# Kernel optimization log

Measured on AMD Instinct MI355X. Metric: run time of the kernel, lower is better.

## Reference

```python
import jax, jax.numpy as jnp
import numpy as np

B, C, N = 4, 128, 25000
E = 200000            # edges per graph
H, DH = 4, 32         # heads, per-head dim
OUT = H * DH          # 128
ED = 32               # edge feature dim


def setup_inputs() -> dict:
    key = jax.random.key(0)
    ks = jax.random.split(key, 16)
    s = 0.05
    return {
        'x': jax.random.normal(ks[0], (B, C, N, 1), jnp.float32),
        'edge_index': jax.random.randint(ks[1], (B, 2, E), 0, B * N, jnp.int64),
        'edge_attr': jax.random.normal(ks[2], (B * E, ED), jnp.float32),
        'Wq': jax.random.normal(ks[3], (C, OUT), jnp.float32) * s,
        'bq': jnp.zeros((OUT,), jnp.float32),
        'Wk': jax.random.normal(ks[4], (C, OUT), jnp.float32) * s,
        'bk': jnp.zeros((OUT,), jnp.float32),
        'Wv': jax.random.normal(ks[5], (C, OUT), jnp.float32) * s,
        'bv': jnp.zeros((OUT,), jnp.float32),
        'We': jax.random.normal(ks[6], (ED, OUT), jnp.float32) * s,
        'Wskip': jax.random.normal(ks[7], (C, OUT), jnp.float32) * s,
        'bskip': jnp.zeros((OUT,), jnp.float32),
        'W1': jax.random.normal(ks[8], (OUT, 2 * OUT), jnp.float32) * s,
        'b1': jnp.zeros((2 * OUT,), jnp.float32),
        'W2': jax.random.normal(ks[9], (2 * OUT, OUT), jnp.float32) * s,
        'b2': jnp.zeros((OUT,), jnp.float32),
    }


def reference(x, edge_index, edge_attr, Wq, bq, Wk, bk, Wv, bv, We,
              Wskip, bskip, W1, b1, W2, b2):
    b, c, n, _ = x.shape
    nb = b * n
    # [B,C,N,1] -> [B*N, C]
    xf = x.squeeze(-1).transpose(0, 2, 1).reshape(nb, c)
    # [B,2,E] -> [2, B*E]
    ei = edge_index.transpose(1, 0, 2).reshape(2, -1)
    src, dst = ei[0], ei[1]

    q = (xf @ Wq + bq).reshape(nb, H, DH)
    k = (xf @ Wk + bk).reshape(nb, H, DH)
    v = (xf @ Wv + bv).reshape(nb, H, DH)
    e = (edge_attr @ We).reshape(-1, H, DH)  # [T,H,DH]

    qi = q[dst]            # gather target queries  [T,H,DH]
    kj = k[src] + e        # gather source keys + edge proj
    vj = v[src] + e

    scale = 1.0 / np.sqrt(DH).astype(np.float32)
    alpha = (qi * kj).sum(-1) * scale  # [T,H]

    # segment softmax over edges sharing a destination node
    amax = jax.ops.segment_max(alpha, dst, num_segments=nb)
    amax = jnp.where(jnp.isfinite(amax), amax, 0.0)
    ea = jnp.exp(alpha - amax[dst])
    denom = jax.ops.segment_sum(ea, dst, num_segments=nb)
    attn = ea / (denom[dst] + 1e-16)   # [T,H]

    agg = jax.ops.segment_sum(vj * attn[..., None], dst, num_segments=nb)
    out = agg.reshape(nb, OUT) + (xf @ Wskip + bskip)  # root skip

    # feed-forward + final activation
    h = jnp.maximum(out @ W1 + b1, 0.0) @ W2 + b2
    h = jnp.maximum(h, 0.0)

    # [B*N, OUT] -> [B, OUT, N, 1]
    return h.reshape(b, n, OUT).transpose(0, 2, 1)[..., None]
```

## Files before the change

### kernel.cpp

```cpp
#include <hip/hip_runtime.h>
#include <hip/hip_bf16.h>

#define NB      100000
#define NPB     25000
#define T_E     800000
#define EPG     200000
#define DMODEL  128
#define EDIM    32
#define FFD     256
#define SCAN_NBLK 98
#define PROJ_BLK  1563
#define HIST_BLK  3125
#define EPROJ_BLK 2048

typedef __attribute__((ext_vector_type(8))) short bf16x8;
typedef __attribute__((ext_vector_type(4))) float f32x4;
typedef __attribute__((ext_vector_type(2))) float f32x2;

__device__ inline unsigned short f2bf(float f) {
    unsigned u = __float_as_uint(f);
    unsigned r = u + 0x7fffu + ((u >> 16) & 1u);
    return (unsigned short)(r >> 16);
}
__device__ inline unsigned pack_bf16x2(float lo, float hi) {
    return (unsigned)f2bf(lo) | ((unsigned)f2bf(hi) << 16);
}
__device__ inline float bf_lo(unsigned p) { return __uint_as_float(p << 16); }
__device__ inline float bf_hi(unsigned p) { return __uint_as_float(p & 0xffff0000u); }

__global__ __launch_bounds__(256) void k_prep(
    const float* __restrict__ W1, const float* __restrict__ W2,
    const float* __restrict__ We,
    const float* __restrict__ Wq, const float* __restrict__ Wk,
    const float* __restrict__ Wv, const float* __restrict__ Wskip,
    uint4* __restrict__ w1f, uint4* __restrict__ w2f,
    uint4* __restrict__ wef, uint4* __restrict__ wpf)
{
    int t = blockIdx.x * 256 + threadIdx.x;
    int lane = t & 63;
    int frag = t >> 6;
    if (frag >= 264) return;
    int rl = lane & 15, g = lane >> 4;
    unsigned v[4];
    if (frag < 64) {
        int m1 = frag >> 2, ks = frag & 3;
        int col1 = m1 * 16 + rl;
        int k0 = ks * 32 + g * 8;
#pragma unroll
        for (int j2 = 0; j2 < 4; ++j2) {
            float f0 = W1[(k0 + 2 * j2) * FFD + col1];
            float f1 = W1[(k0 + 2 * j2 + 1) * FFD + col1];
            v[j2] = pack_bf16x2(f0, f1);
        }
        w1f[frag * 64 + lane] = make_uint4(v[0], v[1], v[2], v[3]);
    } else if (frag < 128) {
        int f2 = frag - 64;
        int m2 = f2 >> 3, ks = f2 & 7;
        int c2 = m2 * 16 + rl;
        int k0 = ks * 32 + g * 8;
#pragma unroll
        for (int j2 = 0; j2 < 4; ++j2) {
            float f0 = W2[(k0 + 2 * j2) * DMODEL + c2];
            float f1 = W2[(k0 + 2 * j2 + 1) * DMODEL + c2];
            v[j2] = pack_bf16x2(f0, f1);
        }
        w2f[f2 * 64 + lane] = make_uint4(v[0], v[1], v[2], v[3]);
    } else if (frag < 136) {
        int m = frag - 128;
        int ocol = m * 16 + rl;
        int k0 = g * 8;
#pragma unroll
        for (int j2 = 0; j2 < 4; ++j2) {
            float f0 = We[(k0 + 2 * j2) * DMODEL + ocol];
            float f1 = We[(k0 + 2 * j2 + 1) * DMODEL + ocol];
            v[j2] = pack_bf16x2(f0, f1);
        }
        wef[m * 64 + lane] = make_uint4(v[0], v[1], v[2], v[3]);
    } else {
        int fi = frag - 136;
        int m  = fi >> 5;
        int r  = fi & 31;
        int ct = r >> 2, ks = r & 3;
        const float* W = (m == 0) ? Wq : (m == 1) ? Wk : (m == 2) ? Wv : Wskip;
        int col = ct * 16 + rl;
        int k0  = ks * 32 + g * 8;
#pragma unroll
        for (int j2 = 0; j2 < 4; ++j2) {
            float f0 = W[(k0 + 2 * j2) * DMODEL + col];
            float f1 = W[(k0 + 2 * j2 + 1) * DMODEL + col];
            v[j2] = pack_bf16x2(f0, f1);
        }
        wpf[fi * 64 + lane] = make_uint4(v[0], v[1], v[2], v[3]);
    }
}

#define STG 16384

__global__ __launch_bounds__(256) void k_projhist(
    const float* __restrict__ x, const uint4* __restrict__ wpf,
    const float* __restrict__ bq, const float* __restrict__ bk,
    const float* __restrict__ bv, const float* __restrict__ bskip,
    unsigned short* __restrict__ qb16, unsigned short* __restrict__ kvb,
    unsigned short* __restrict__ skipb16,
    const int* __restrict__ eidx, int* __restrict__ counts)
{
    __shared__ __align__(16) char lds[32768];
    const int tid = threadIdx.x;

    if (blockIdx.x >= PROJ_BLK) {
        int t = (blockIdx.x - PROJ_BLK) * 256 + tid;
        if (t < T_E) {
            int b = t / EPG, e = t - b * EPG;
            int dst = eidx[(size_t)(b * 2 + 1) * EPG + e];
            atomicAdd(&counts[dst], 1);
        }
        return;
    }

    const int node0 = blockIdx.x * 64;

    {
        const int nl   = tid & 63;
        const int half = tid >> 6;
        const int node = node0 + nl;
        const bool valid = node < NB;
        int b  = node / NPB;
        int nn = node - b * NPB;
        const float* xbase = x + (size_t)b * DMODEL * NPB + nn;
#pragma unroll
        for (int o = 0; o < 4; ++o) {
            int c0 = (half * 4 + o) * 8;
            unsigned vals[4];
#pragma unroll
            for (int j2 = 0; j2 < 4; ++j2) {
                float f0 = valid ? xbase[(size_t)(c0 + 2 * j2) * NPB] : 0.f;
                float f1 = valid ? xbase[(size_t)(c0 + 2 * j2 + 1) * NPB] : 0.f;
                vals[j2] = pack_bf16x2(f0, f1);
            }
            int byte = nl * 256 + ((c0 * 2) ^ ((nl & 7) << 4));
            *(uint4*)(&lds[byte]) = make_uint4(vals[0], vals[1], vals[2], vals[3]);
        }
    }
    __syncthreads();

    const int w = tid >> 6, lane = tid & 63;
    const int rl = lane & 15, g = lane >> 4;

    for (int m = 0; m < 4; ++m) {
        const float* bi = (m == 0) ? bq : (m == 1) ? bk : (m == 2) ? bv : bskip;
#pragma unroll
        for (int ct2 = 0; ct2 < 2; ++ct2) {
            const int ct = w * 2 + ct2;
            bf16x8 A[4];
#pragma unroll
            for (int ks = 0; ks < 4; ++ks)
                A[ks] = *(const bf16x8*)&wpf[((m * 8 + ct) * 4 + ks) * 64 + lane];
            const int colb = ct * 16 + g * 4;
            const float bb0 = bi[colb], bb1 = bi[colb + 1],
                        bb2 = bi[colb + 2], bb3 = bi[colb + 3];
#pragma unroll
            for (int nt = 0; nt < 4; ++nt) {
                const int nl = nt * 16 + rl;
                f32x4 acc = {0.f, 0.f, 0.f, 0.f};
#pragma unroll
                for (int ks = 0; ks < 4; ++ks) {
                    bf16x8 B = *(const bf16x8*)(&lds[nl * 256 +
                                  ((ks * 64 + g * 16) ^ ((nl & 7) << 4))]);
                    acc = __builtin_amdgcn_mfma_f32_16x16x32_bf16(A[ks], B, acc, 0, 0, 0);
                }
                unsigned lo = pack_bf16x2(acc[0] + bb0, acc[1] + bb1);
                unsigned hi = pack_bf16x2(acc[2] + bb2, acc[3] + bb3);
                int byte = STG + nl * 256 + ((colb * 2) ^ ((nl & 7) << 4));
                *(uint2*)(&lds[byte]) = make_uint2(lo, hi);
            }
        }
        __syncthreads();
#pragma unroll
        for (int i = 0; i < 4; ++i) {
            int linear = i * 256 + tid;
            int row = linear >> 4;
            int c8  = (linear & 15) * 8;
            int node = node0 + row;
            if (node < NB) {
                uint4 vv = *(const uint4*)(&lds[STG + row * 256 +
                                ((c8 * 2) ^ ((row & 7) << 4))]);
                if (m == 0)      *(uint4*)&qb16[(size_t)node * DMODEL + c8] = vv;
                else if (m == 1) *(uint4*)&kvb[(size_t)node * 256 + c8] = vv;
                else if (m == 2) *(uint4*)&kvb[(size_t)node * 256 + 128 + c8] = vv;
                else             *(uint4*)&skipb16[(size_t)node * DMODEL + c8] = vv;
            }
        }
        __syncthreads();
    }
}

__global__ __launch_bounds__(1024) void k_scan1(
    const int* __restrict__ counts, int* __restrict__ row_start,
    int* __restrict__ bsum)
{
    __shared__ int s[1024];
    const int tid = threadIdx.x;
    const int gid = blockIdx.x * 1024 + tid;
    int v = (gid < NB) ? counts[gid] : 0;
    s[tid] = v;
    __syncthreads();
#pragma unroll
    for (int off = 1; off < 1024; off <<= 1) {
        int tv = (tid >= off) ? s[tid - off] : 0;
        __syncthreads();
        s[tid] += tv;
        __syncthreads();
    }
    int incl = s[tid];
    if (gid < NB) row_start[gid] = incl - v;
    if (tid == 1023) bsum[blockIdx.x] = incl;
}

__global__ __launch_bounds__(128) void k_scan2(int* __restrict__ bsum)
{
    __shared__ int s[128];
    const int tid = threadIdx.x;
    int v = (tid < SCAN_NBLK) ? bsum[tid] : 0;
    s[tid] = v;
    __syncthreads();
#pragma unroll
    for (int off = 1; off < 128; off <<= 1) {
        int tv = (tid >= off) ? s[tid - off] : 0;
        __syncthreads();
        s[tid] += tv;
        __syncthreads();
    }
    if (tid < SCAN_NBLK) bsum[tid] = s[tid] - v;
}

__global__ __launch_bounds__(1024) void k_scan3(
    int* __restrict__ row_start, const int* __restrict__ bsum,
    int* __restrict__ cursor)
{
    const int gid = blockIdx.x * 1024 + threadIdx.x;
    if (gid < NB) {
        int v = row_start[gid] + bsum[blockIdx.x];
        row_start[gid] = v;
        cursor[gid] = v;
    }
}

__global__ __launch_bounds__(256) void k_escat2(
    const float* __restrict__ eattr, const uint4* __restrict__ wef,
    unsigned char* __restrict__ eb,
    const int* __restrict__ eidx, int* __restrict__ cursor,
    int2* __restrict__ elist2)
{
    __shared__ __align__(16) char elds[8192];
    const int tid = threadIdx.x;

    if (blockIdx.x >= EPROJ_BLK) {
        int t = (blockIdx.x - EPROJ_BLK) * 256 + tid;
        if (t < T_E) {
            int b = t / EPG, e = t - b * EPG;
            int dst = eidx[(size_t)(b * 2 + 1) * EPG + e];
            int src = eidx[(size_t)(b * 2) * EPG + e];
            int pos = atomicAdd(&cursor[dst], 1);
            elist2[pos] = make_int2(src, t);
        }
        return;
    }

    const int w = tid >> 6, lane = tid & 63;
    const int rl = lane & 15, g = lane >> 4;
    char* myl = &elds[w * 2048];

    bf16x8 a[8];
#pragma unroll
    for (int m = 0; m < 8; ++m) a[m] = *(const bf16x8*)&wef[m * 64 + lane];

    const int nwaves = EPROJ_BLK * 4;
    for (int tile = blockIdx.x * 4 + w; tile < T_E / 16; tile += nwaves) {
        const float* ep = &eattr[((size_t)tile * 16 + rl) * EDIM + g * 8];
        float4 f0 = *(const float4*)ep;
        float4 f1 = *(const float4*)(ep + 4);
        uint4 bu = make_uint4(pack_bf16x2(f0.x, f0.y), pack_bf16x2(f0.z, f0.w),
                              pack_bf16x2(f1.x, f1.y), pack_bf16x2(f1.z, f1.w));
        bf16x8 b = *(bf16x8*)&bu;
        f32x4 z = {0.f, 0.f, 0.f, 0.f};
        f32x4 acc[8];
#pragma unroll
        for (int m = 0; m < 8; ++m)
            acc[m] = __builtin_amdgcn_mfma_f32_16x16x32_bf16(a[m], b, z, 0, 0, 0);
#pragma unroll
        for (int m = 0; m < 8; ++m) {
            unsigned d = __builtin_amdgcn_cvt_pk_fp8_f32(acc[m][0], acc[m][1], 0, false);
            d = __builtin_amdgcn_cvt_pk_fp8_f32(acc[m][2], acc[m][3], d, true);
            *(unsigned*)(myl + rl * 128 + ((m * 16) ^ ((rl & 7) << 4)) + g * 4) = d;
        }
#pragma unroll
        for (int it = 0; it < 2; ++it) {
            int lin = it * 64 + lane;
            int row = lin >> 3, chunk = lin & 7;
            uint4 vv = *(const uint4*)(myl + row * 128 + ((chunk ^ (row & 7)) << 4));
            *(uint4*)&eb[(size_t)tile * 2048 + (size_t)lin * 16] = vv;
        }
    }
}

__global__ __launch_bounds__(256) void k_aggr3(
    unsigned short* qx,
    const unsigned short* __restrict__ kvb,
    const unsigned short* __restrict__ skipb16,
    const unsigned char* __restrict__ eb,
    const int2* __restrict__ elist2,
    const int* __restrict__ row_start, const int* __restrict__ row_end)
{
    const int tid = threadIdx.x;
    const int w = tid >> 6, l = tid & 63;
    const int q4 = l >> 4;
    const int li = l & 15;
    const int c0 = li * 8;

    const int nwaves = gridDim.x * 4;
    for (int node = blockIdx.x * 4 + w; node < NB; node += nwaves) {
        const int rs = row_start[node];
        const int re = row_end[node];
        uint4 qp = *(const uint4*)&qx[(size_t)node * DMODEL + c0];
        const float q0 = bf_lo(qp.x), q1 = bf_hi(qp.x);
        const float q2 = bf_lo(qp.y), q3 = bf_hi(qp.y);
        const float q4_ = bf_lo(qp.z), q5 = bf_hi(qp.z);
        const float q6 = bf_lo(qp.w), q7 = bf_hi(qp.w);
        float a0 = 0.f, a1 = 0.f, a2 = 0.f, a3 = 0.f;
        float a4 = 0.f, a5 = 0.f, a6 = 0.f, a7 = 0.f, den = 0.f;

        for (int j0 = rs; j0 < re; j0 += 8) {
            const int jcA = j0 + q4;
            const int jcB = j0 + 4 + q4;
            const bool actA = jcA < re;
            const bool actB = jcB < re;
            uint4 kpA = make_uint4(0,0,0,0), vpA = make_uint4(0,0,0,0);
            uint4 kpB = make_uint4(0,0,0,0), vpB = make_uint4(0,0,0,0);
            uint2 epA = make_uint2(0,0), epB = make_uint2(0,0);
            if (actA) {
                int2 se = elist2[jcA];
                kpA = *(const uint4*)&kvb[(size_t)se.x * 256 + c0];
                vpA = *(const uint4*)&kvb[(size_t)se.x * 256 + 128 + c0];
                epA = *(const uint2*)&eb[(size_t)se.y * DMODEL + c0];
            }
            if (actB) {
                int2 se = elist2[jcB];
                kpB = *(const uint4*)&kvb[(size_t)se.x * 256 + c0];
                vpB = *(const uint4*)&kvb[(size_t)se.x * 256 + 128 + c0];
                epB = *(const uint2*)&eb[(size_t)se.y * DMODEL + c0];
            }
            {
                f32x2 exl = __builtin_amdgcn_cvt_pk_f32_fp8(epA.x, false);
                f32x2 exh = __builtin_amdgcn_cvt_pk_f32_fp8(epA.x, true);
                f32x2 eyl = __builtin_amdgcn_cvt_pk_f32_fp8(epA.y, false);
                f32x2 eyh = __builtin_amdgcn_cvt_pk_f32_fp8(epA.y, true);
                const float e0 = exl[0], e1 = exl[1], e2 = exh[0], e3 = exh[1];
                const float e4 = eyl[0], e5 = eyl[1], e6 = eyh[0], e7 = eyh[1];
                float p = q0 * (bf_lo(kpA.x) + e0) + q1 * (bf_hi(kpA.x) + e1)
                        + q2 * (bf_lo(kpA.y) + e2) + q3 * (bf_hi(kpA.y) + e3)
                        + q4_ * (bf_lo(kpA.z) + e4) + q5 * (bf_hi(kpA.z) + e5)
                        + q6 * (bf_lo(kpA.w) + e6) + q7 * (bf_hi(kpA.w) + e7);
                p += __shfl_xor(p, 1, 64);
                p += __shfl_xor(p, 2, 64);
                float ea = actA ? __expf(p * 0.17677669529663689f) : 0.f;
                a0 += ea * (bf_lo(vpA.x) + e0);  a1 += ea * (bf_hi(vpA.x) + e1);
                a2 += ea * (bf_lo(vpA.y) + e2);  a3 += ea * (bf_hi(vpA.y) + e3);
                a4 += ea * (bf_lo(vpA.z) + e4);  a5 += ea * (bf_hi(vpA.z) + e5);
                a6 += ea * (bf_lo(vpA.w) + e6);  a7 += ea * (bf_hi(vpA.w) + e7);
                den += ea;
            }
            {
                f32x2 exl = __builtin_amdgcn_cvt_pk_f32_fp8(epB.x, false);
                f32x2 exh = __builtin_amdgcn_cvt_pk_f32_fp8(epB.x, true);
                f32x2 eyl = __builtin_amdgcn_cvt_pk_f32_fp8(epB.y, false);
                f32x2 eyh = __builtin_amdgcn_cvt_pk_f32_fp8(epB.y, true);
                const float e0 = exl[0], e1 = exl[1], e2 = exh[0], e3 = exh[1];
                const float e4 = eyl[0], e5 = eyl[1], e6 = eyh[0], e7 = eyh[1];
                float p = q0 * (bf_lo(kpB.x) + e0) + q1 * (bf_hi(kpB.x) + e1)
                        + q2 * (bf_lo(kpB.y) + e2) + q3 * (bf_hi(kpB.y) + e3)
                        + q4_ * (bf_lo(kpB.z) + e4) + q5 * (bf_hi(kpB.z) + e5)
                        + q6 * (bf_lo(kpB.w) + e6) + q7 * (bf_hi(kpB.w) + e7);
                p += __shfl_xor(p, 1, 64);
                p += __shfl_xor(p, 2, 64);
                float ea = actB ? __expf(p * 0.17677669529663689f) : 0.f;
                a0 += ea * (bf_lo(vpB.x) + e0);  a1 += ea * (bf_hi(vpB.x) + e1);
                a2 += ea * (bf_lo(vpB.y) + e2);  a3 += ea * (bf_hi(vpB.y) + e3);
                a4 += ea * (bf_lo(vpB.z) + e4);  a5 += ea * (bf_hi(vpB.z) + e5);
                a6 += ea * (bf_lo(vpB.w) + e6);  a7 += ea * (bf_hi(vpB.w) + e7);
                den += ea;
            }
        }
#pragma unroll
        for (int off = 16; off <= 32; off <<= 1) {
            a0 += __shfl_xor(a0, off, 64);  a1 += __shfl_xor(a1, off, 64);
            a2 += __shfl_xor(a2, off, 64);  a3 += __shfl_xor(a3, off, 64);
            a4 += __shfl_xor(a4, off, 64);  a5 += __shfl_xor(a5, off, 64);
            a6 += __shfl_xor(a6, off, 64);  a7 += __shfl_xor(a7, off, 64);
            den += __shfl_xor(den, off, 64);
        }
        float r = 1.0f / (den + 1e-16f);
        if (q4 == 0) {
            uint4 sp = *(const uint4*)&skipb16[(size_t)node * DMODEL + c0];
            uint4 o;
            o.x = pack_bf16x2(a0 * r + bf_lo(sp.x), a1 * r + bf_hi(sp.x));
            o.y = pack_bf16x2(a2 * r + bf_lo(sp.y), a3 * r + bf_hi(sp.y));
            o.z = pack_bf16x2(a4 * r + bf_lo(sp.z), a5 * r + bf_hi(sp.z));
            o.w = pack_bf16x2(a6 * r + bf_lo(sp.w), a7 * r + bf_hi(sp.w));
            *(uint4*)&qx[(size_t)node * DMODEL + c0] = o;
        }
    }
}

#define H1_OFF 16384

__global__ __launch_bounds__(256) void k_ffn_mfma(
    const unsigned short* __restrict__ xs16,
    const uint4* __restrict__ w1f, const float* __restrict__ b1,
    const uint4* __restrict__ w2f, const float* __restrict__ b2,
    float* __restrict__ out)
{
    __shared__ __align__(16) char lds[49152];
    const int tid   = threadIdx.x;
    const int node0 = blockIdx.x * 64;

#pragma unroll
    for (int i = 0; i < 4; ++i) {
        int linear = i * 256 + tid;
        int row = linear >> 4;
        int c8  = (linear & 15) * 8;
        int node = node0 + row;
        uint4 vv = (node < NB) ? *(const uint4*)&xs16[(size_t)node * DMODEL + c8]
                               : make_uint4(0, 0, 0, 0);
        int byte = row * 256 + ((c8 * 2) ^ ((row & 7) << 4));
        *(uint4*)(&lds[byte]) = vv;
    }
    __syncthreads();

    const int w = tid >> 6, lane = tid & 63;
    const int rl = lane & 15, g = lane >> 4;

    {
        f32x4 acc[4][4] = {};
#pragma unroll
        for (int ks = 0; ks < 4; ++ks) {
            bf16x8 a[4], b[4];
#pragma unroll
            for (int mt = 0; mt < 4; ++mt) {
                int m1 = w * 4 + mt;
                a[mt] = *(const bf16x8*)&w1f[(m1 * 4 + ks) * 64 + lane];
            }
#pragma unroll
            for (int nt = 0; nt < 4; ++nt) {
                int node = nt * 16 + rl;
                int byte = node * 256 + ((ks * 64 + g * 16) ^ ((node & 7) << 4));
                b[nt] = *(const bf16x8*)&lds[byte];
            }
#pragma unroll
            for (int mt = 0; mt < 4; ++mt)
#pragma unroll
                for (int nt = 0; nt < 4; ++nt)
                    acc[mt][nt] = __builtin_amdgcn_mfma_f32_16x16x32_bf16(
                        a[mt], b[nt], acc[mt][nt], 0, 0, 0);
        }
#pragma unroll
        for (int mt = 0; mt < 4; ++mt) {
            int col1_0 = w * 64 + mt * 16 + g * 4;
            float bb0 = b1[col1_0], bb1 = b1[col1_0 + 1],
                  bb2 = b1[col1_0 + 2], bb3 = b1[col1_0 + 3];
#pragma unroll
            for (int nt = 0; nt < 4; ++nt) {
                int node = nt * 16 + rl;
                float v0 = fmaxf(acc[mt][nt][0] + bb0, 0.f);
                float v1 = fmaxf(acc[mt][nt][1] + bb1, 0.f);
                float v2 = fmaxf(acc[mt][nt][2] + bb2, 0.f);
                float v3 = fmaxf(acc[mt][nt][3] + bb3, 0.f);
                unsigned lo = pack_bf16x2(v0, v1), hi = pack_bf16x2(v2, v3);
                int byte = H1_OFF + node * 512 + ((col1_0 * 2) ^ ((node & 7) << 4));
                *(uint2*)(&lds[byte]) = make_uint2(lo, hi);
            }
        }
    }
    __syncthreads();

    {
        f32x4 acc[2][4] = {};
#pragma unroll
        for (int ks = 0; ks < 8; ++ks) {
            bf16x8 a[2], b[4];
#pragma unroll
            for (int mt = 0; mt < 2; ++mt) {
                int m2 = w * 2 + mt;
                a[mt] = *(const bf16x8*)&w2f[(m2 * 8 + ks) * 64 + lane];
            }
#pragma unroll
            for (int nt = 0; nt < 4; ++nt) {
                int node = nt * 16 + rl;
                int byte = H1_OFF + node * 512 + ((ks * 64 + g * 16) ^ ((node & 7) << 4));
                b[nt] = *(const bf16x8*)&lds[byte];
            }
#pragma unroll
            for (int mt = 0; mt < 2; ++mt)
#pragma unroll
                for (int nt = 0; nt < 4; ++nt)
                    acc[mt][nt] = __builtin_amdgcn_mfma_f32_16x16x32_bf16(
                        a[mt], b[nt], acc[mt][nt], 0, 0, 0);
        }
#pragma unroll
        for (int mt = 0; mt < 2; ++mt) {
            int c2_0 = w * 32 + mt * 16 + g * 4;
#pragma unroll
            for (int nt = 0; nt < 4; ++nt) {
                int node = node0 + nt * 16 + rl;
                if (node < NB) {
                    int bb = node / NPB;
                    int nn = node - bb * NPB;
                    size_t base = (size_t)(bb * DMODEL) * NPB + nn;
#pragma unroll
                    for (int r = 0; r < 4; ++r) {
                        float v = fmaxf(acc[mt][nt][r] + b2[c2_0 + r], 0.f);
                        out[base + (size_t)(c2_0 + r) * NPB] = v;
                    }
                }
            }
        }
    }
}

extern "C" void kernel_launch(void* const* d_in, const int* in_sizes, int n_in,
                              void* d_out, int out_size, void* d_ws, size_t ws_size,
                              hipStream_t stream)
{
    const float* x     = (const float*)d_in[0];
    const int*   eidx  = (const int*)  d_in[1];
    const float* eattr = (const float*)d_in[2];
    const float* Wq    = (const float*)d_in[3];
    const float* bq    = (const float*)d_in[4];
    const float* Wk    = (const float*)d_in[5];
    const float* bk    = (const float*)d_in[6];
    const float* Wv    = (const float*)d_in[7];
    const float* bv    = (const float*)d_in[8];
    const float* We    = (const float*)d_in[9];
    const float* Wskip = (const float*)d_in[10];
    const float* bskip = (const float*)d_in[11];
    const float* W1    = (const float*)d_in[12];
    const float* b1    = (const float*)d_in[13];
    const float* W2    = (const float*)d_in[14];
    const float* b2    = (const float*)d_in[15];
    float* out = (float*)d_out;

    const size_t NBD = (size_t)NB * DMODEL;
    unsigned short* qb16    = (unsigned short*)d_ws;
    unsigned short* kvb     = qb16 + NBD;
    unsigned short* skipb16 = kvb + 2 * NBD;
    unsigned char*  eb      = (unsigned char*)(skipb16 + NBD);
    uint4* w1f = (uint4*)(eb + (size_t)T_E * DMODEL);
    uint4* w2f = w1f + 64 * 64;
    uint4* wef = w2f + 64 * 64;
    uint4* wpf = wef + 8 * 64;
    int* counts    = (int*)(wpf + 128 * 64);
    int* row_start = counts + NB;
    int* cursor    = row_start + NB;
    int2* elist2   = (int2*)(cursor + NB);
    int* bsum      = (int*)(elist2 + T_E);

    hipMemsetAsync(counts, 0, NB * sizeof(int), stream);
    k_prep<<<66, 256, 0, stream>>>(W1, W2, We, Wq, Wk, Wv, Wskip,
                                   w1f, w2f, wef, wpf);
    k_projhist<<<PROJ_BLK + HIST_BLK, 256, 0, stream>>>(
        x, wpf, bq, bk, bv, bskip, qb16, kvb, skipb16, eidx, counts);
    k_scan1<<<SCAN_NBLK, 1024, 0, stream>>>(counts, row_start, bsum);
    k_scan2<<<1, 128, 0, stream>>>(bsum);
    k_scan3<<<SCAN_NBLK, 1024, 0, stream>>>(row_start, bsum, cursor);
    k_escat2<<<EPROJ_BLK + HIST_BLK, 256, 0, stream>>>(
        eattr, wef, eb, eidx, cursor, elist2);
    k_aggr3<<<2048, 256, 0, stream>>>(qb16, kvb, skipb16, eb, elist2,
                                      row_start, cursor);
    k_ffn_mfma<<<(NB + 63) / 64, 256, 0, stream>>>(qb16, w1f, b1, w2f, b2, out);
}
```

Measured before the change: 306.5 us.

## Move edge-feature projection into node-projection/histogram kernel with interleaved block roles

The edge-attribute projection (MFMA to fp8) moves out of the scatter kernel into the first phase kernel, which now assigns node projection, edge projection and histogram work to blocks interleaved by blockIdx modulo 4. The scatter kernel becomes a plain atomic-cursor scatter. The edge projection loop also prefetches the next tile's attributes one iteration ahead. The aim is to overlap the bandwidth-heavy edge projection with the node projection and histogram, which do not depend on the prefix scan, and to shorten the serial chain after the scan. The cost is a larger fused launch with many early-exit blocks and a more complex role-dispatch kernel.

```diff
diff --git a/kernel.cpp b/kernel.cpp
--- a/kernel.cpp
+++ b/kernel.cpp
@@ -10,8 +10,9 @@
 #define FFD     256
 #define SCAN_NBLK 98
 #define PROJ_BLK  1563
-#define HIST_BLK  3125
-#define EPROJ_BLK 2048
+#define NT_E      50000
+#define PHA_GRP   1584
+#define PHA_BLK   (PHA_GRP * 4)
 
 typedef __attribute__((ext_vector_type(8))) short bf16x8;
 typedef __attribute__((ext_vector_type(4))) float f32x4;
@@ -96,19 +97,23 @@
 
 #define STG 16384
 
-__global__ __launch_bounds__(256) void k_projhist(
+__global__ __launch_bounds__(256) void k_phaseA(
     const float* __restrict__ x, const uint4* __restrict__ wpf,
     const float* __restrict__ bq, const float* __restrict__ bk,
     const float* __restrict__ bv, const float* __restrict__ bskip,
     unsigned short* __restrict__ qb16, unsigned short* __restrict__ kvb,
     unsigned short* __restrict__ skipb16,
+    const float* __restrict__ eattr, const uint4* __restrict__ wef,
+    unsigned char* __restrict__ eb,
     const int* __restrict__ eidx, int* __restrict__ counts)
 {
     __shared__ __align__(16) char lds[32768];
-    const int tid = threadIdx.x;
-
-    if (blockIdx.x >= PROJ_BLK) {
-        int t = (blockIdx.x - PROJ_BLK) * 256 + tid;
+    const int tid  = threadIdx.x;
+    const int role = blockIdx.x & 3;
+
+    if (role >= 2) {
+        int hid = (blockIdx.x >> 2) * 2 + (blockIdx.x & 1);
+        int t = hid * 256 + tid;
         if (t < T_E) {
             int b = t / EPG, e = t - b * EPG;
             int dst = eidx[(size_t)(b * 2 + 1) * EPG + e];
@@ -117,7 +122,60 @@
         return;
     }
 
-    const int node0 = blockIdx.x * 64;
+    const int w = tid >> 6, lane = tid & 63;
+    const int rl = lane & 15, g = lane >> 4;
+
+    if (role == 1) {
+        char* myl = &lds[w * 2048];
+        bf16x8 a[8];
+#pragma unroll
+        for (int m = 0; m < 8; ++m) a[m] = *(const bf16x8*)&wef[m * 64 + lane];
+
+        const int stride = PHA_GRP * 4;
+        int tile = (blockIdx.x >> 2) * 4 + w;
+        if (tile >= NT_E) return;
+        const float* ep = &eattr[((size_t)tile * 16 + rl) * EDIM + g * 8];
+        float4 f0 = *(const float4*)ep;
+        float4 f1 = *(const float4*)(ep + 4);
+        while (tile < NT_E) {
+            int tnext = tile + stride;
+            float4 nf0, nf1;
+            if (tnext < NT_E) {
+                const float* np = &eattr[((size_t)tnext * 16 + rl) * EDIM + g * 8];
+                nf0 = *(const float4*)np;
+                nf1 = *(const float4*)(np + 4);
+            }
+            uint4 bu = make_uint4(pack_bf16x2(f0.x, f0.y), pack_bf16x2(f0.z, f0.w),
+                                  pack_bf16x2(f1.x, f1.y), pack_bf16x2(f1.z, f1.w));
+            bf16x8 b = *(bf16x8*)&bu;
+            f32x4 z = {0.f, 0.f, 0.f, 0.f};
+            f32x4 acc[8];
+#pragma unroll
+            for (int m = 0; m < 8; ++m)
+                acc[m] = __builtin_amdgcn_mfma_f32_16x16x32_bf16(a[m], b, z, 0, 0, 0);
+#pragma unroll
+            for (int m = 0; m < 8; ++m) {
+                unsigned d = __builtin_amdgcn_cvt_pk_fp8_f32(acc[m][0], acc[m][1], 0, false);
+                d = __builtin_amdgcn_cvt_pk_fp8_f32(acc[m][2], acc[m][3], d, true);
+                *(unsigned*)(myl + rl * 128 + ((m * 16) ^ ((rl & 7) << 4)) + g * 4) = d;
+            }
+#pragma unroll
+            for (int it = 0; it < 2; ++it) {
+                int lin = it * 64 + lane;
+                int row = lin >> 3, chunk = lin & 7;
+                uint4 vv = *(const uint4*)(myl + row * 128 + ((chunk ^ (row & 7)) << 4));
+                *(uint4*)&eb[(size_t)tile * 2048 + (size_t)lin * 16] = vv;
+            }
+            tile = tnext;
+            f0 = nf0;
+            f1 = nf1;
+        }
+        return;
+    }
+
+    const int pid = blockIdx.x >> 2;
+    if (pid >= PROJ_BLK) return;
+    const int node0 = pid * 64;
 
     {
         const int nl   = tid & 63;
@@ -142,9 +200,6 @@
         }
     }
     __syncthreads();
-
-    const int w = tid >> 6, lane = tid & 63;
-    const int rl = lane & 15, g = lane >> 4;
 
     for (int m = 0; m < 4; ++m) {
         const float* bi = (m == 0) ? bq : (m == 1) ? bk : (m == 2) ? bv : bskip;
@@ -245,61 +300,17 @@
     }
 }
 
-__global__ __launch_bounds__(256) void k_escat2(
-    const float* __restrict__ eattr, const uint4* __restrict__ wef,
-    unsigned char* __restrict__ eb,
+__global__ __launch_bounds__(256) void k_scatter(
     const int* __restrict__ eidx, int* __restrict__ cursor,
     int2* __restrict__ elist2)
 {
-    __shared__ __align__(16) char elds[8192];
-    const int tid = threadIdx.x;
-
-    if (blockIdx.x >= EPROJ_BLK) {
-        int t = (blockIdx.x - EPROJ_BLK) * 256 + tid;
-        if (t < T_E) {
-            int b = t / EPG, e = t - b * EPG;
-            int dst = eidx[(size_t)(b * 2 + 1) * EPG + e];
-            int src = eidx[(size_t)(b * 2) * EPG + e];
-            int pos = atomicAdd(&cursor[dst], 1);
-            elist2[pos] = make_int2(src, t);
-        }
-        return;
-    }
-
-    const int w = tid >> 6, lane = tid & 63;
-    const int rl = lane & 15, g = lane >> 4;
-    char* myl = &elds[w * 2048];
-
-    bf16x8 a[8];
-#pragma unroll
-    for (int m = 0; m < 8; ++m) a[m] = *(const bf16x8*)&wef[m * 64 + lane];
-
-    const int nwaves = EPROJ_BLK * 4;
-    for (int tile = blockIdx.x * 4 + w; tile < T_E / 16; tile += nwaves) {
-        const float* ep = &eattr[((size_t)tile * 16 + rl) * EDIM + g * 8];
-        float4 f0 = *(const float4*)ep;
-        float4 f1 = *(const float4*)(ep + 4);
-        uint4 bu = make_uint4(pack_bf16x2(f0.x, f0.y), pack_bf16x2(f0.z, f0.w),
-                              pack_bf16x2(f1.x, f1.y), pack_bf16x2(f1.z, f1.w));
-        bf16x8 b = *(bf16x8*)&bu;
-        f32x4 z = {0.f, 0.f, 0.f, 0.f};
-        f32x4 acc[8];
-#pragma unroll
-        for (int m = 0; m < 8; ++m)
-            acc[m] = __builtin_amdgcn_mfma_f32_16x16x32_bf16(a[m], b, z, 0, 0, 0);
-#pragma unroll
-        for (int m = 0; m < 8; ++m) {
-            unsigned d = __builtin_amdgcn_cvt_pk_fp8_f32(acc[m][0], acc[m][1], 0, false);
-            d = __builtin_amdgcn_cvt_pk_fp8_f32(acc[m][2], acc[m][3], d, true);
-            *(unsigned*)(myl + rl * 128 + ((m * 16) ^ ((rl & 7) << 4)) + g * 4) = d;
-        }
-#pragma unroll
-        for (int it = 0; it < 2; ++it) {
-            int lin = it * 64 + lane;
-            int row = lin >> 3, chunk = lin & 7;
-            uint4 vv = *(const uint4*)(myl + row * 128 + ((chunk ^ (row & 7)) << 4));
-            *(uint4*)&eb[(size_t)tile * 2048 + (size_t)lin * 16] = vv;
-        }
+    int t = blockIdx.x * 256 + threadIdx.x;
+    if (t < T_E) {
+        int b = t / EPG, e = t - b * EPG;
+        int dst = eidx[(size_t)(b * 2 + 1) * EPG + e];
+        int src = eidx[(size_t)(b * 2) * EPG + e];
+        int pos = atomicAdd(&cursor[dst], 1);
+        elist2[pos] = make_int2(src, t);
     }
 }
 
@@ -566,13 +577,13 @@
     hipMemsetAsync(counts, 0, NB * sizeof(int), stream);
     k_prep<<<66, 256, 0, stream>>>(W1, W2, We, Wq, Wk, Wv, Wskip,
                                    w1f, w2f, wef, wpf);
-    k_projhist<<<PROJ_BLK + HIST_BLK, 256, 0, stream>>>(
-        x, wpf, bq, bk, bv, bskip, qb16, kvb, skipb16, eidx, counts);
+    k_phaseA<<<PHA_BLK, 256, 0, stream>>>(
+        x, wpf, bq, bk, bv, bskip, qb16, kvb, skipb16,
+        eattr, wef, eb, eidx, counts);
     k_scan1<<<SCAN_NBLK, 1024, 0, stream>>>(counts, row_start, bsum);
     k_scan2<<<1, 128, 0, stream>>>(bsum);
     k_scan3<<<SCAN_NBLK, 1024, 0, stream>>>(row_start, bsum, cursor);
-    k_escat2<<<EPROJ_BLK + HIST_BLK, 256, 0, stream>>>(
-        eattr, wef, eb, eidx, cursor, elist2);
+    k_scatter<<<(T_E + 255) / 256, 256, 0, stream>>>(eidx, cursor, elist2);
     k_aggr3<<<2048, 256, 0, stream>>>(qb16, kvb, skipb16, eb, elist2,
                                       row_start, cursor);
     k_ffn_mfma<<<(NB + 63) / 64, 256, 0, stream>>>(qb16, w1f, b1, w2f, b2, out);
```

Result: slower. 332.1 us (+8.4%).
